# Performance work log

Measured on AMD Instinct MI355X. Metric: run time of the kernel, lower is better.

Reference implementation:

```python
import jax, jax.numpy as jnp
import numpy as np

N = 8192      # nodes (= hidden_channels / heads)
E = 262144    # edges (avg degree 32)
IN = 256      # in_channels
H = 8         # heads
C = 32        # out_channels per head
NEG_SLOPE = 0.2


def setup_inputs() -> dict:
    key = jax.random.key(0)
    ks = jax.random.split(key, 8)
    x = jax.random.normal(ks[0], (N, IN), jnp.float32)
    edge_index = jax.random.randint(ks[1], (2, E), 0, N, dtype=jnp.int32)
    lin_w = jax.random.normal(ks[2], (H * C, IN), jnp.float32) * (1.0 / np.sqrt(IN))
    att_src = jax.random.normal(ks[3], (H, C), jnp.float32) * 0.1
    att_dst = jax.random.normal(ks[4], (H, C), jnp.float32) * 0.1
    bias = jax.random.normal(ks[5], (H * C,), jnp.float32) * 0.01
    out_w = jax.random.normal(ks[6], (C, N * H * C), jnp.float32) * (1.0 / np.sqrt(N * H * C))
    out_b = jax.random.normal(ks[7], (C,), jnp.float32) * 0.01
    return {"x": x, "edge_index": edge_index, "lin_w": lin_w, "att_src": att_src,
            "att_dst": att_dst, "bias": bias, "out_w": out_w, "out_b": out_b}


def reference(x, edge_index, lin_w, att_src, att_dst, bias, out_w, out_b):
    n = x.shape[0]
    # PyG GATConv default: add self loops
    loop = jnp.arange(n, dtype=edge_index.dtype)
    src = jnp.concatenate([edge_index[0], loop])  # message sources j
    dst = jnp.concatenate([edge_index[1], loop])  # message targets i
    # per-head linear projection: [n, H, C]
    xh = (x @ lin_w.T).reshape(n, H, C)
    a_src = jnp.einsum('nhc,hc->nh', xh, att_src)  # [n, H]
    a_dst = jnp.einsum('nhc,hc->nh', xh, att_dst)  # [n, H]
    # edge attention logits + segment softmax over incoming edges of each dst
    e = jax.nn.leaky_relu(a_src[src] + a_dst[dst], negative_slope=NEG_SLOPE)  # [E', H]
    m = jax.ops.segment_max(e, dst, num_segments=n)        # [n, H]
    ex = jnp.exp(e - m[dst])
    denom = jax.ops.segment_sum(ex, dst, num_segments=n)   # [n, H]
    alpha = ex / denom[dst]                                 # [E', H]
    # weighted scatter-add aggregation
    agg = jax.ops.segment_sum(alpha[:, :, None] * xh[src], dst, num_segments=n)  # [n, H, C]
    out = agg.reshape(n, H * C) + bias
    # flatten all nodes, dense output layer, softmax
    y = out.reshape(-1) @ out_w.T + out_b  # [C]
    return jax.nn.softmax(y)
```

## Files before the change

kernel.cpp:

```cpp
#include <hip/hip_runtime.h>


namespace {
constexpr int  kN    = 8192;
constexpr int  kE    = 262144;
constexpr int  kTotE = kE + kN;
constexpr long kK    = 2097152;
constexpr int  kYB   = 256;
}

typedef float vfloat4 __attribute__((ext_vector_type(4)));

static __device__ __forceinline__ ushort f2bf(float f) {
  unsigned u = __float_as_uint(f);
  return (ushort)((u + 0x7FFFu + ((u >> 16) & 1u)) >> 16);
}
static __device__ __forceinline__ float bf2f(ushort b) {
  return __uint_as_float(((unsigned)b) << 16);
}

__global__ __launch_bounds__(256) void gemm_att_hist(const float* __restrict__ x,
                                                     const float* __restrict__ lw,
                                                     const float* __restrict__ att_s,
                                                     const float* __restrict__ att_d,
                                                     const int* __restrict__ ei,
                                                     ushort* __restrict__ xh_bf,
                                                     float* __restrict__ a_src,
                                                     float* __restrict__ a_dst,
                                                     int* __restrict__ cnt) {
  __shared__ float As[16][68];
  __shared__ float Bs[16][68];
  const int t  = threadIdx.x;
  const int tx = t & 15, ty = t >> 4;
  const int rowBase = blockIdx.x * 64;
  const int colBase = blockIdx.y * 64;
  const int lr = t >> 2;
  const int lk = (t & 3) * 4;

  {
    const int bid = blockIdx.y * 128 + blockIdx.x;
    const int gid = bid * 512 + t;
    atomicAdd(&cnt[ei[kE + gid]], 1);
    atomicAdd(&cnt[ei[kE + gid + 256]], 1);
  }

  float acc[4][4] = {};
  for (int kc = 0; kc < 256; kc += 16) {
    float4 av = *(const float4*)(x  + (long)(rowBase + lr) * 256 + kc + lk);
    float4 bv = *(const float4*)(lw + (long)(colBase + lr) * 256 + kc + lk);
    __syncthreads();
    As[lk + 0][lr] = av.x; As[lk + 1][lr] = av.y; As[lk + 2][lr] = av.z; As[lk + 3][lr] = av.w;
    Bs[lk + 0][lr] = bv.x; Bs[lk + 1][lr] = bv.y; Bs[lk + 2][lr] = bv.z; Bs[lk + 3][lr] = bv.w;
    __syncthreads();
#pragma unroll
    for (int k = 0; k < 16; k++) {
      float4 a4 = *(const float4*)(&As[k][ty * 4]);
      float4 b4 = *(const float4*)(&Bs[k][tx * 4]);
      float aa[4] = {a4.x, a4.y, a4.z, a4.w};
      float bb[4] = {b4.x, b4.y, b4.z, b4.w};
#pragma unroll
      for (int i = 0; i < 4; i++)
#pragma unroll
        for (int j = 0; j < 4; j++) acc[i][j] += aa[i] * bb[j];
    }
  }

#pragma unroll
  for (int i = 0; i < 4; i++) {
    const long row = rowBase + ty * 4 + i;
    ushort4 ob = make_ushort4(f2bf(acc[i][0]), f2bf(acc[i][1]),
                              f2bf(acc[i][2]), f2bf(acc[i][3]));
    *(ushort4*)(xh_bf + row * 256 + colBase + tx * 4) = ob;
  }

  float4 as4 = *(const float4*)(att_s + colBase + tx * 4);
  float4 ad4 = *(const float4*)(att_d + colBase + tx * 4);
#pragma unroll
  for (int i = 0; i < 4; i++) {
    float s = acc[i][0] * as4.x + acc[i][1] * as4.y + acc[i][2] * as4.z + acc[i][3] * as4.w;
    float d = acc[i][0] * ad4.x + acc[i][1] * ad4.y + acc[i][2] * ad4.z + acc[i][3] * ad4.w;
#pragma unroll
    for (int off = 4; off; off >>= 1) {
      s += __shfl_down(s, off, 8);
      d += __shfl_down(d, off, 8);
    }
    if ((tx & 7) == 0) {
      const int row  = rowBase + ty * 4 + i;
      const int head = blockIdx.y * 2 + (tx >> 3);
      a_src[row * 8 + head] = s;
      a_dst[row * 8 + head] = d;
    }
  }
}

__global__ __launch_bounds__(1024) void scan_cnt(const int* __restrict__ cnt,
                                                 int* __restrict__ rowptr,
                                                 int* __restrict__ wpos) {
  __shared__ int wsum[16];
  const int t = threadIdx.x, lane = t & 63, w = t >> 6;
  int v[8]; int sum = 0;
#pragma unroll
  for (int q = 0; q < 8; q++) { v[q] = cnt[t * 8 + q] + 1; sum += v[q]; }
  int sc = sum;
#pragma unroll
  for (int off = 1; off < 64; off <<= 1) {
    int n = __shfl_up(sc, off, 64);
    if (lane >= off) sc += n;
  }
  if (lane == 63) wsum[w] = sc;
  __syncthreads();
  if (t < 16) {
    int ws = wsum[t];
#pragma unroll
    for (int off = 1; off < 16; off <<= 1) {
      int n = __shfl_up(ws, off, 16);
      if ((t & 15) >= off) ws += n;
    }
    wsum[t] = ws;
  }
  __syncthreads();
  int excl = (w ? wsum[w - 1] : 0) + sc - sum;
#pragma unroll
  for (int q = 0; q < 8; q++) {
    rowptr[t * 8 + q] = excl;
    wpos[t * 8 + q]   = excl;
    excl += v[q];
  }
  if (t == 1023) rowptr[kN] = excl;
}

__global__ __launch_bounds__(256) void scatter_csr(const int* __restrict__ ei,
                                                   const float* __restrict__ a_src,
                                                   const float* __restrict__ a_dst,
                                                   int* __restrict__ wpos,
                                                   int* __restrict__ csr,
                                                   float* __restrict__ w8) {
  int idx = blockIdx.x * 256 + threadIdx.x;
  if (idx >= kTotE) return;
  int s, d;
  if (idx < kE) { s = ei[idx]; d = ei[kE + idx]; }
  else          { s = idx - kE; d = s; }
  int pos = atomicAdd(&wpos[d], 1);
  csr[pos] = s;
  float4 s0 = *(const float4*)(a_src + s * 8);
  float4 s1 = *(const float4*)(a_src + s * 8 + 4);
  float4 d0 = *(const float4*)(a_dst + d * 8);
  float4 d1 = *(const float4*)(a_dst + d * 8 + 4);
  float e[8] = {s0.x + d0.x, s0.y + d0.y, s0.z + d0.z, s0.w + d0.w,
                s1.x + d1.x, s1.y + d1.y, s1.z + d1.z, s1.w + d1.w};
  float w[8];
#pragma unroll
  for (int h = 0; h < 8; h++) {
    float ee = (e[h] > 0.f) ? e[h] : 0.2f * e[h];
    w[h] = __expf(ee);
  }
  float4* wp = (float4*)(w8 + (long)pos * 8);
  wp[0] = make_float4(w[0], w[1], w[2], w[3]);
  wp[1] = make_float4(w[4], w[5], w[6], w[7]);
}

__global__ __launch_bounds__(256) void agg_dot(const ushort* __restrict__ xb,
                                               const float* __restrict__ w8,
                                               const int* __restrict__ rowptr,
                                               const int* __restrict__ csr,
                                               const float* __restrict__ bias,
                                               const float* __restrict__ w,
                                               float* __restrict__ ypart) {
  const int i = blockIdx.x, t = threadIdx.x, h = t >> 5;
  const int lane = t & 63, wid = t >> 6;

  const int beg = rowptr[i], end = rowptr[i + 1];

  const long wbase = (long)i * 256 + lane * 4;
  vfloat4 wv[8];
#pragma unroll
  for (int cc = 0; cc < 8; cc++) {
    const int c = cc * 4 + wid;
    wv[cc] = __builtin_nontemporal_load((const vfloat4*)(w + (long)c * kK + wbase));
  }

  float acc = 0.f, den = 0.f;
  for (int j = beg; j < end; j += 8) {
    const int lim = end - j;
    int s[8]; float ww[8]; float f[8];
#pragma unroll
    for (int q = 0; q < 8; q++) {
      const int jj = (q < lim) ? j + q : j;
      s[q]  = csr[jj];
      ww[q] = w8[(long)jj * 8 + h];
    }
#pragma unroll
    for (int q = 0; q < 8; q++) f[q] = bf2f(xb[(long)s[q] * 256 + t]);
#pragma unroll
    for (int q = 0; q < 8; q++) {
      const float wq = (q < lim) ? ww[q] : 0.f;
      den += wq;
      acc += wq * f[q];
    }
  }

  __shared__ float ofs[256];
  __shared__ float yb[32];
  ofs[t] = acc / den + bias[t];
  __syncthreads();
  float4 f4 = *(const float4*)(ofs + lane * 4);
#pragma unroll
  for (int cc = 0; cc < 8; cc++) {
    float p = wv[cc].x * f4.x + wv[cc].y * f4.y + wv[cc].z * f4.z + wv[cc].w * f4.w;
    p += __shfl_down(p, 32, 64);
    p += __shfl_down(p, 16, 64);
    p += __shfl_down(p, 8, 64);
    p += __shfl_down(p, 4, 64);
    p += __shfl_down(p, 2, 64);
    p += __shfl_down(p, 1, 64);
    if (lane == 0) yb[cc * 4 + wid] = p;
  }
  __syncthreads();
  if (t < 32) atomicAdd(&ypart[(i & (kYB - 1)) * 32 + t], yb[t]);
}

__global__ __launch_bounds__(1024) void finalize(const float* __restrict__ ypart,
                                                 const float* __restrict__ ob,
                                                 float* __restrict__ out) {
  __shared__ float s[32][33];
  const int t = threadIdx.x;
  const int c = t & 31, r = t >> 5;
  float sum = 0.f;
  for (int q = r; q < kYB; q += 32) sum += ypart[q * 32 + c];
  s[c][r] = sum;
  __syncthreads();
  if (t < 32) {
    float y = ob[t];
#pragma unroll
    for (int r2 = 0; r2 < 32; r2++) y += s[t][r2];
    float m = y;
#pragma unroll
    for (int off = 16; off; off >>= 1) m = fmaxf(m, __shfl_xor(m, off, 32));
    float e = __expf(y - m);
    float d = e;
#pragma unroll
    for (int off = 16; off; off >>= 1) d += __shfl_xor(d, off, 32);
    out[t] = e / d;
  }
}

extern "C" void kernel_launch(void* const* d_in, const int* in_sizes, int n_in,
                              void* d_out, int out_size, void* d_ws, size_t ws_size,
                              hipStream_t stream) {
  (void)in_sizes; (void)n_in; (void)out_size; (void)ws_size;
  const float* x     = (const float*)d_in[0];
  const int*   ei    = (const int*)  d_in[1];
  const float* lin_w = (const float*)d_in[2];
  const float* att_s = (const float*)d_in[3];
  const float* att_d = (const float*)d_in[4];
  const float* bias  = (const float*)d_in[5];
  const float* out_w = (const float*)d_in[6];
  const float* out_b = (const float*)d_in[7];
  float* out = (float*)d_out;

  float*  a_src    = (float*)d_ws;
  float*  a_dst    = a_src + kN * 8;
  float*  w8       = a_dst + kN * 8;
  ushort* xh_bf    = (ushort*)(w8 + (long)kTotE * 8);
  int*    cnt      = (int*)(xh_bf + kK);
  float*  ypart    = (float*)(cnt + kN);
  int*    rowptr   = (int*)(ypart + kYB * 32);
  int*    wpos     = rowptr + (kN + 1);
  int*    csr      = wpos + kN;

  (void)hipMemsetAsync(cnt, 0, kN * sizeof(int) + kYB * 32 * sizeof(float), stream);
  gemm_att_hist<<<dim3(128, 4), 256, 0, stream>>>(x, lin_w, att_s, att_d, ei,
                                                  xh_bf, a_src, a_dst, cnt);
  scan_cnt   <<<1, 1024, 0, stream>>>(cnt, rowptr, wpos);
  scatter_csr<<<(kTotE + 255) / 256, 256, 0, stream>>>(ei, a_src, a_dst, wpos, csr, w8);
  agg_dot    <<<kN, 256, 0, stream>>>(xh_bf, w8, rowptr, csr, bias, out_w, ypart);
  finalize   <<<1, 1024, 0, stream>>>(ypart, out_b, out);
}
```

Baseline: 426.1 us.

## Use split-bf16 MFMA (3-pass) for the projection GEMM in gemm_att_hist

Replaces the scalar FP32 register-tiled GEMM with bf16 MFMA 16x16x32 instructions. Each FP32 operand is split into high and low bf16 parts, and three MFMA products are accumulated to keep near-FP32 accuracy. Results are staged through shared memory so the existing bf16 store and attention-dot epilogue can reuse them. The intent is to cut the projection GEMM's compute time, at the cost of more LDS traffic, conversion work and an extra LDS round trip; this GEMM is only one part of the whole pipeline.

```diff
diff --git a/kernel.cpp b/kernel.cpp
--- a/kernel.cpp
+++ b/kernel.cpp
@@ -10,6 +10,8 @@
 }
 
 typedef float vfloat4 __attribute__((ext_vector_type(4)));
+typedef short bf16x8  __attribute__((ext_vector_type(8)));
+typedef float f32x4   __attribute__((ext_vector_type(4)));
 
 static __device__ __forceinline__ ushort f2bf(float f) {
   unsigned u = __float_as_uint(f);
@@ -17,6 +19,10 @@
 }
 static __device__ __forceinline__ float bf2f(ushort b) {
   return __uint_as_float(((unsigned)b) << 16);
+}
+static __device__ __forceinline__ void bfsplit(float f, ushort& h, ushort& l) {
+  h = f2bf(f);
+  l = f2bf(f - bf2f(h));
 }
 
 __global__ __launch_bounds__(256) void gemm_att_hist(const float* __restrict__ x,
@@ -28,14 +34,11 @@
                                                      float* __restrict__ a_src,
                                                      float* __restrict__ a_dst,
                                                      int* __restrict__ cnt) {
-  __shared__ float As[16][68];
-  __shared__ float Bs[16][68];
+  __shared__ __align__(16) ushort AB[4][64][136];
   const int t  = threadIdx.x;
-  const int tx = t & 15, ty = t >> 4;
   const int rowBase = blockIdx.x * 64;
   const int colBase = blockIdx.y * 64;
-  const int lr = t >> 2;
-  const int lk = (t & 3) * 4;
+  const int lane = t & 63, wv = t >> 6;
 
   {
     const int bid = blockIdx.y * 128 + blockIdx.x;
@@ -44,48 +47,69 @@
     atomicAdd(&cnt[ei[kE + gid + 256]], 1);
   }
 
-  float acc[4][4] = {};
-  for (int kc = 0; kc < 256; kc += 16) {
-    float4 av = *(const float4*)(x  + (long)(rowBase + lr) * 256 + kc + lk);
-    float4 bv = *(const float4*)(lw + (long)(colBase + lr) * 256 + kc + lk);
+  f32x4 acc[4] = {};
+
+  for (int kc = 0; kc < 256; kc += 128) {
     __syncthreads();
-    As[lk + 0][lr] = av.x; As[lk + 1][lr] = av.y; As[lk + 2][lr] = av.z; As[lk + 3][lr] = av.w;
-    Bs[lk + 0][lr] = bv.x; Bs[lk + 1][lr] = bv.y; Bs[lk + 2][lr] = bv.z; Bs[lk + 3][lr] = bv.w;
+#pragma unroll
+    for (int i2 = 0; i2 < 8; i2++) {
+      const int s = t + 256 * i2;
+      const int r = s >> 5, c4 = s & 31;
+      float4 xa = *(const float4*)(x  + (long)(rowBase + r) * 256 + kc + c4 * 4);
+      float4 ba = *(const float4*)(lw + (long)(colBase + r) * 256 + kc + c4 * 4);
+      ushort4 xh4, xl4, bh4, bl4;
+      bfsplit(xa.x, xh4.x, xl4.x); bfsplit(xa.y, xh4.y, xl4.y);
+      bfsplit(xa.z, xh4.z, xl4.z); bfsplit(xa.w, xh4.w, xl4.w);
+      bfsplit(ba.x, bh4.x, bl4.x); bfsplit(ba.y, bh4.y, bl4.y);
+      bfsplit(ba.z, bh4.z, bl4.z); bfsplit(ba.w, bh4.w, bl4.w);
+      *(ushort4*)&AB[0][r][c4 * 4] = xh4;
+      *(ushort4*)&AB[1][r][c4 * 4] = xl4;
+      *(ushort4*)&AB[2][r][c4 * 4] = bh4;
+      *(ushort4*)&AB[3][r][c4 * 4] = bl4;
+    }
     __syncthreads();
 #pragma unroll
-    for (int k = 0; k < 16; k++) {
-      float4 a4 = *(const float4*)(&As[k][ty * 4]);
-      float4 b4 = *(const float4*)(&Bs[k][tx * 4]);
-      float aa[4] = {a4.x, a4.y, a4.z, a4.w};
-      float bb[4] = {b4.x, b4.y, b4.z, b4.w};
-#pragma unroll
-      for (int i = 0; i < 4; i++)
-#pragma unroll
-        for (int j = 0; j < 4; j++) acc[i][j] += aa[i] * bb[j];
-    }
-  }
-
+    for (int ks = 0; ks < 4; ks++) {
+      const int ko = ks * 32 + ((lane >> 4) << 3);
+      bf16x8 ah = *(const bf16x8*)&AB[0][wv * 16 + (lane & 15)][ko];
+      bf16x8 al = *(const bf16x8*)&AB[1][wv * 16 + (lane & 15)][ko];
+#pragma unroll
+      for (int ct = 0; ct < 4; ct++) {
+        bf16x8 bh = *(const bf16x8*)&AB[2][ct * 16 + (lane & 15)][ko];
+        bf16x8 bl = *(const bf16x8*)&AB[3][ct * 16 + (lane & 15)][ko];
+        acc[ct] = __builtin_amdgcn_mfma_f32_16x16x32_bf16(ah, bh, acc[ct], 0, 0, 0);
+        acc[ct] = __builtin_amdgcn_mfma_f32_16x16x32_bf16(al, bh, acc[ct], 0, 0, 0);
+        acc[ct] = __builtin_amdgcn_mfma_f32_16x16x32_bf16(ah, bl, acc[ct], 0, 0, 0);
+      }
+    }
+  }
+  __syncthreads();
+
+  float (*Ds)[68] = reinterpret_cast<float(*)[68]>(&AB[0][0][0]);
+#pragma unroll
+  for (int ct = 0; ct < 4; ct++)
+#pragma unroll
+    for (int r = 0; r < 4; r++)
+      Ds[wv * 16 + ((lane >> 4) << 2) + r][ct * 16 + (lane & 15)] = acc[ct][r];
+  __syncthreads();
+
+  const int tx = t & 15, ty = t >> 4;
+  float4 as4 = *(const float4*)(att_s + colBase + tx * 4);
+  float4 ad4 = *(const float4*)(att_d + colBase + tx * 4);
 #pragma unroll
   for (int i = 0; i < 4; i++) {
     const long row = rowBase + ty * 4 + i;
-    ushort4 ob = make_ushort4(f2bf(acc[i][0]), f2bf(acc[i][1]),
-                              f2bf(acc[i][2]), f2bf(acc[i][3]));
+    float4 v = *(const float4*)&Ds[ty * 4 + i][tx * 4];
+    ushort4 ob = make_ushort4(f2bf(v.x), f2bf(v.y), f2bf(v.z), f2bf(v.w));
     *(ushort4*)(xh_bf + row * 256 + colBase + tx * 4) = ob;
-  }
-
-  float4 as4 = *(const float4*)(att_s + colBase + tx * 4);
-  float4 ad4 = *(const float4*)(att_d + colBase + tx * 4);
-#pragma unroll
-  for (int i = 0; i < 4; i++) {
-    float s = acc[i][0] * as4.x + acc[i][1] * as4.y + acc[i][2] * as4.z + acc[i][3] * as4.w;
-    float d = acc[i][0] * ad4.x + acc[i][1] * ad4.y + acc[i][2] * ad4.z + acc[i][3] * ad4.w;
+    float s = v.x * as4.x + v.y * as4.y + v.z * as4.z + v.w * as4.w;
+    float d = v.x * ad4.x + v.y * ad4.y + v.z * ad4.z + v.w * ad4.w;
 #pragma unroll
     for (int off = 4; off; off >>= 1) {
       s += __shfl_down(s, off, 8);
       d += __shfl_down(d, off, 8);
     }
     if ((tx & 7) == 0) {
-      const int row  = rowBase + ty * 4 + i;
       const int head = blockIdx.y * 2 + (tx >> 3);
       a_src[row * 8 + head] = s;
       a_dst[row * 8 + head] = d;
```

Result: faster. 415.8 us (-2.4%).
